# Performance work log

Measured on AMD Instinct MI355X. Metric: run time of the kernel, lower is better.

## Reference

```python
import jax, jax.numpy as jnp
import numpy as np

N_NODES = 50000
N_EDGES = 800000
F_IN = 128
HID = 128
HID4 = HID // 4  # 32
N_SEL = 8192


def gcn_conv(x, src, dst, norm, W, b, n_nodes):
    h = x @ W                              # [N, out]
    msg = h[src] * norm[:, None]           # gather + scale, [E+N, out]
    out = jax.ops.segment_sum(msg, dst, num_segments=n_nodes)  # scatter-add
    return out + b


def setup_inputs() -> dict:
    key = jax.random.key(0)
    ks = jax.random.split(key, 12)
    def glorot(k, shape):
        lim = np.sqrt(6.0 / (shape[0] + shape[1])).astype(np.float32)
        return jax.random.uniform(k, shape, jnp.float32, -lim, lim)
    return {
        "x": jax.random.normal(ks[0], (N_NODES, F_IN), jnp.float32),
        "edge_index": jax.random.randint(ks[1], (2, N_EDGES), 0, N_NODES, jnp.int64 if jax.config.jax_enable_x64 else jnp.int32),
        "relevant_batch_indices": jax.random.randint(ks[2], (N_SEL,), 0, N_NODES),
        "labels": jax.random.randint(ks[3], (N_SEL,), 0, 2),
        "W1": glorot(ks[4], (F_IN, HID)),   "b1": jnp.zeros((HID,), jnp.float32),
        "W2": glorot(ks[5], (HID, HID4)),   "b2": jnp.zeros((HID4,), jnp.float32),
        "W3": glorot(ks[6], (HID4, HID4)),  "b3": jnp.zeros((HID4,), jnp.float32),
        "Wl": glorot(ks[7], (HID4, 2)),     "bl": jnp.zeros((2,), jnp.float32),
    }


def reference(x, edge_index, relevant_batch_indices, labels, W1, b1, W2, b2, W3, b3, Wl, bl):
    n = x.shape[0]
    loops = jnp.arange(n, dtype=edge_index.dtype)
    src = jnp.concatenate([edge_index[0], loops])  # add self-loops
    dst = jnp.concatenate([edge_index[1], loops])
    deg = jax.ops.segment_sum(jnp.ones_like(dst, dtype=x.dtype), dst, num_segments=n)
    dis = jnp.where(deg > 0, jax.lax.rsqrt(jnp.maximum(deg, 1e-12)), 0.0)
    norm = dis[src] * dis[dst]             # [E+N]

    h = jax.nn.relu(gcn_conv(x, src, dst, norm, W1, b1, n))
    h = jax.nn.relu(gcn_conv(h, src, dst, norm, W2, b2, n))
    h = gcn_conv(h, src, dst, norm, W3, b3, n)

    logits = h[relevant_batch_indices] @ Wl + bl   # [N_SEL, 2]
    softmax_vals = jax.nn.softmax(logits, axis=1)
    lsm = jax.nn.log_softmax(logits, axis=1)
    # original slices lsm to labels length if longer; here shapes match
    lsm = lsm[: labels.shape[0]]
    return (lsm, softmax_vals)
```

## Files before the change

kernel.cpp:

```cpp
#include <hip/hip_runtime.h>
#include <hip/hip_fp16.h>

#define F_IN 128
#define HID 128
#define HID4 32
#define NPB 256
#define SRC_BITS 17
#define NBK 256
#define MAXBUCKET 256

static inline size_t alignup(size_t x) { return (x + 255) & ~(size_t)255; }

typedef _Float16 half8 __attribute__((ext_vector_type(8)));
typedef float f32x4 __attribute__((ext_vector_type(4)));

union F4H8 { float4 f; __half2 h[4]; };
union U2H4 { uint2 u; _Float16 h[4]; };


__global__ __launch_bounds__(1024) void hist_k(const int* __restrict__ dst,
                                               int* __restrict__ ghist,
                                               const float* __restrict__ W1,
                                               _Float16* __restrict__ Wt,
                                               int ne, int n_buckets) {
    __shared__ int h[MAXBUCKET];
    const int t = threadIdx.x;
    if (blockIdx.x < 16) {
        int q = blockIdx.x * 1024 + t;
        int k = q >> 7, n = q & 127;
        Wt[n * 128 + k] = (_Float16)W1[q];
    }
    for (int b = t; b < n_buckets; b += 1024) h[b] = 0;
    __syncthreads();
    const int chunk = (ne + NBK - 1) / NBK;
    const int beg = blockIdx.x * chunk;
    const int end = min(ne, beg + chunk);
    for (int e = beg + t; e < end; e += 1024)
        atomicAdd(&h[dst[e] / NPB], 1);
    __syncthreads();
    for (int b = t; b < n_buckets; b += 1024)
        ghist[(size_t)b * NBK + blockIdx.x] = h[b];
}


__global__ void scan_block_k(const int* __restrict__ in, int* __restrict__ out,
                             int* __restrict__ partials, int n) {
    __shared__ int tmp[256];
    int i = blockIdx.x * 256 + threadIdx.x;
    int v = (i < n) ? in[i] : 0;
    tmp[threadIdx.x] = v;
    __syncthreads();
    for (int off = 1; off < 256; off <<= 1) {
        int t = (threadIdx.x >= off) ? tmp[threadIdx.x - off] : 0;
        __syncthreads();
        tmp[threadIdx.x] += t;
        __syncthreads();
    }
    if (i < n) out[i] = tmp[threadIdx.x] - v;
    if (threadIdx.x == 255) partials[blockIdx.x] = tmp[255];
}

__global__ void scan_partials_k(int* __restrict__ partials, int nb) {
    __shared__ int tmp[256];
    int v = (threadIdx.x < nb) ? partials[threadIdx.x] : 0;
    tmp[threadIdx.x] = v;
    __syncthreads();
    for (int off = 1; off < 256; off <<= 1) {
        int t = (threadIdx.x >= off) ? tmp[threadIdx.x - off] : 0;
        __syncthreads();
        tmp[threadIdx.x] += t;
        __syncthreads();
    }
    if (threadIdx.x < nb) partials[threadIdx.x] = tmp[threadIdx.x] - v;
}


__global__ __launch_bounds__(1024) void fused_scatter_gemm1_k(
        const int* __restrict__ src, const int* __restrict__ dst,
        const int* __restrict__ goff, const int* __restrict__ partial2,
        unsigned* __restrict__ tmp, int ne, int n_buckets,
        const float* __restrict__ in, const _Float16* __restrict__ Wt,
        __half* __restrict__ hout, int n_rows) {
    __shared__ int cur[MAXBUCKET];
    __shared__ _Float16 xs[64][136];
    const int t = threadIdx.x;

    if (blockIdx.x < NBK) {
        for (int b = t; b < n_buckets; b += 1024)
            cur[b] = goff[(size_t)b * NBK + blockIdx.x] + partial2[b];
        __syncthreads();
        const int chunk = (ne + NBK - 1) / NBK;
        const int beg = blockIdx.x * chunk;
        const int end = min(ne, beg + chunk);
        for (int e = beg + t; e < end; e += 1024) {
            int d = dst[e];
            int s = src[e];
            int pos = atomicAdd(&cur[d / NPB], 1);
            tmp[pos] = ((unsigned)(d & (NPB - 1)) << SRC_BITS) | (unsigned)s;
        }
        return;
    }

    const int row0 = (blockIdx.x - NBK) * 64;

    #pragma unroll
    for (int i = 0; i < 2; ++i) {
        int q = t + i * 1024;
        int row = q >> 5, c4 = (q & 31) * 4;
        float4 v = make_float4(0.f, 0.f, 0.f, 0.f);
        if (row0 + row < n_rows) v = *(const float4*)(in + (size_t)(row0 + row) * 128 + c4);
        U2H4 cv;
        cv.h[0] = (_Float16)v.x; cv.h[1] = (_Float16)v.y;
        cv.h[2] = (_Float16)v.z; cv.h[3] = (_Float16)v.w;
        *(uint2*)&xs[row][c4] = cv.u;
    }
    __syncthreads();

    const int lane = t & 63;
    const int wave = t >> 6;
    const int r0 = (wave & 3) * 16;
    const int cg = (wave >> 2) * 32;
    const int lrow = lane & 15;
    const int kgrp = (lane >> 4) * 8;

    f32x4 acc[2];
    acc[0] = (f32x4){0.f, 0.f, 0.f, 0.f};
    acc[1] = (f32x4){0.f, 0.f, 0.f, 0.f};

    #pragma unroll
    for (int kk = 0; kk < 4; ++kk) {
        const int k0 = kk * 32 + kgrp;
        half8 a = *(const half8*)&xs[r0 + lrow][k0];
        #pragma unroll
        for (int ct = 0; ct < 2; ++ct) {
            half8 b = *(const half8*)(Wt + (size_t)(cg + ct * 16 + lrow) * 128 + k0);
            acc[ct] = __builtin_amdgcn_mfma_f32_16x16x32_f16(a, b, acc[ct], 0, 0, 0);
        }
    }

    const int rbase = row0 + r0 + (lane >> 4) * 4;
    #pragma unroll
    for (int i = 0; i < 4; ++i) {
        int row = row0 + r0 + (lane >> 4) * 4 + i;
        if (row < n_rows) {
            __half* p = hout + (size_t)row * 128 + cg + lrow;
            p[0]  = __float2half(acc[0][i]);
            p[16] = __float2half(acc[1][i]);
        }
    }
    (void)rbase;
}


__global__ __launch_bounds__(NPB) void binC_k(const unsigned* __restrict__ tmp,
                                              const int* __restrict__ goff,
                                              const int* __restrict__ partial2,
                                              int* __restrict__ deg, float* __restrict__ dis,
                                              int* __restrict__ rowoff, int* __restrict__ csr,
                                              int n_nodes, int ne, int n_buckets) {
    __shared__ int cnt[NPB];
    __shared__ int sc[NPB];
    const int t = threadIdx.x;
    const int bid = blockIdx.x;
    const int base = goff[(size_t)bid * NBK] + partial2[bid];
    const int end = (bid + 1 < n_buckets) ? goff[(size_t)(bid + 1) * NBK] + partial2[bid + 1] : ne;

    cnt[t] = 0;
    __syncthreads();
    for (int j = base + t; j < end; j += NPB)
        atomicAdd(&cnt[tmp[j] >> SRC_BITS], 1);
    __syncthreads();

    int mydeg = cnt[t];
    sc[t] = mydeg;
    __syncthreads();
    for (int off = 1; off < NPB; off <<= 1) {
        int v = (t >= off) ? sc[t - off] : 0;
        __syncthreads();
        sc[t] += v;
        __syncthreads();
    }
    int excl = sc[t] - mydeg;
    int node = bid * NPB + t;
    if (node < n_nodes) {
        deg[node] = mydeg;
        dis[node] = rsqrtf((float)(mydeg + 1));
        rowoff[node] = base + excl;
    }
    cnt[t] = base + excl;
    __syncthreads();
    for (int j = base + t; j < end; j += NPB) {
        unsigned e = tmp[j];
        int ld = e >> SRC_BITS;
        int s  = e & ((1u << SRC_BITS) - 1);
        int pos = atomicAdd(&cnt[ld], 1);
        csr[pos] = s;
    }
}


__global__ void pull1_k(const __half* __restrict__ g, const int* __restrict__ rowoff,
                        const int* __restrict__ deg, const int* __restrict__ csr,
                        const float* __restrict__ dis, const float* __restrict__ b,
                        __half* __restrict__ out, int n_nodes) {
    int gt = blockIdx.x * blockDim.x + threadIdx.x;
    int node = gt >> 4;
    int f0 = (gt & 15) * 8;
    if (node >= n_nodes) return;
    int beg = rowoff[node];
    int end = beg + deg[node];
    float dd = dis[node];

    float acc[8];
    {
        F4H8 v; v.f = *(const float4*)(g + (size_t)node * 128 + f0);
        #pragma unroll
        for (int k = 0; k < 4; ++k) {
            float2 p = __half22float2(v.h[k]);
            acc[2 * k] = dd * p.x; acc[2 * k + 1] = dd * p.y;
        }
    }

    int j = beg;
    for (; j + 2 <= end; j += 2) {
        int s0 = csr[j];
        int s1 = csr[j + 1];
        float w0 = dis[s0];
        float w1 = dis[s1];
        F4H8 v0; v0.f = *(const float4*)(g + (size_t)s0 * 128 + f0);
        F4H8 v1; v1.f = *(const float4*)(g + (size_t)s1 * 128 + f0);
        #pragma unroll
        for (int k = 0; k < 4; ++k) {
            float2 p0 = __half22float2(v0.h[k]);
            float2 p1 = __half22float2(v1.h[k]);
            acc[2 * k]     += w0 * p0.x + w1 * p1.x;
            acc[2 * k + 1] += w0 * p0.y + w1 * p1.y;
        }
    }
    if (j < end) {
        int s = csr[j];
        float w = dis[s];
        F4H8 v; v.f = *(const float4*)(g + (size_t)s * 128 + f0);
        #pragma unroll
        for (int k = 0; k < 4; ++k) {
            float2 p = __half22float2(v.h[k]);
            acc[2 * k] += w * p.x; acc[2 * k + 1] += w * p.y;
        }
    }

    float4 b0 = *(const float4*)(b + f0);
    float4 b1 = *(const float4*)(b + f0 + 4);
    F4H8 o;
    o.h[0] = __floats2half2_rn(fmaxf(b0.x + dd * acc[0], 0.f), fmaxf(b0.y + dd * acc[1], 0.f));
    o.h[1] = __floats2half2_rn(fmaxf(b0.z + dd * acc[2], 0.f), fmaxf(b0.w + dd * acc[3], 0.f));
    o.h[2] = __floats2half2_rn(fmaxf(b1.x + dd * acc[4], 0.f), fmaxf(b1.y + dd * acc[5], 0.f));
    o.h[3] = __floats2half2_rn(fmaxf(b1.z + dd * acc[6], 0.f), fmaxf(b1.w + dd * acc[7], 0.f));
    *(float4*)(out + (size_t)node * 128 + f0) = o.f;
}


__global__ __launch_bounds__(256) void gemm2_k(const __half* __restrict__ in,
                                               const float* __restrict__ W,
                                               const float* __restrict__ dis,
                                               __half* __restrict__ out, int n_rows) {
    __shared__ float xs[64][132];
    __shared__ float wt[128][32];
    const int t = threadIdx.x;
    const int row0 = blockIdx.x * 64;

    #pragma unroll
    for (int i = 0; i < 4; ++i) {
        int q = t + i * 256;
        int row = q >> 4, c8 = (q & 15) * 8;
        F4H8 v;
        v.f = make_float4(0.f, 0.f, 0.f, 0.f);
        if (row0 + row < n_rows)
            v.f = *(const float4*)(in + (size_t)(row0 + row) * 128 + c8);
        #pragma unroll
        for (int k = 0; k < 4; ++k) {
            float2 p = __half22float2(v.h[k]);
            xs[row][c8 + 2 * k] = p.x;
            xs[row][c8 + 2 * k + 1] = p.y;
        }
    }
    #pragma unroll
    for (int i = 0; i < 4; ++i) {
        int q = t + i * 256;
        int kk = q >> 3, c4 = (q & 7) * 4;
        *(float4*)&wt[kk][c4] = *(const float4*)(W + (size_t)kk * 32 + c4);
    }
    __syncthreads();

    const int c4 = (t & 7) * 4;
    const int r2 = (t >> 3) * 2;

    float acc[2][4];
    #pragma unroll
    for (int i = 0; i < 2; ++i)
        #pragma unroll
        for (int j = 0; j < 4; ++j) acc[i][j] = 0.f;

    #pragma unroll 4
    for (int k = 0; k < 128; ++k) {
        float x0 = xs[r2][k], x1 = xs[r2 + 1][k];
        float4 w = *(float4*)&wt[k][c4];
        acc[0][0] += x0 * w.x; acc[0][1] += x0 * w.y; acc[0][2] += x0 * w.z; acc[0][3] += x0 * w.w;
        acc[1][0] += x1 * w.x; acc[1][1] += x1 * w.y; acc[1][2] += x1 * w.z; acc[1][3] += x1 * w.w;
    }

    #pragma unroll
    for (int i = 0; i < 2; ++i) {
        int row = row0 + r2 + i;
        if (row < n_rows) {
            float sc = dis[row];
            U2H4 cv;
            cv.h[0] = (_Float16)(sc * acc[i][0]);
            cv.h[1] = (_Float16)(sc * acc[i][1]);
            cv.h[2] = (_Float16)(sc * acc[i][2]);
            cv.h[3] = (_Float16)(sc * acc[i][3]);
            *(uint2*)(out + (size_t)row * 32 + c4) = cv.u;
        }
    }
}


__global__ void pull2_k(const __half* __restrict__ g, const int* __restrict__ rowoff,
                        const int* __restrict__ deg, const int* __restrict__ csr,
                        const float* __restrict__ dis, const float* __restrict__ b,
                        float* __restrict__ out, int n_nodes) {
    int gt = blockIdx.x * blockDim.x + threadIdx.x;
    int node = gt >> 3;
    int f0 = (gt & 7) * 4;
    if (node >= n_nodes) return;
    int beg = rowoff[node];
    int end = beg + deg[node];
    float dd = dis[node];

    float acc[4];
    {
        U2H4 v; v.u = *(const uint2*)(g + (size_t)node * 32 + f0);
        #pragma unroll
        for (int k = 0; k < 4; ++k) acc[k] = (float)v.h[k];
    }

    int j = beg;
    for (; j + 2 <= end; j += 2) {
        int s0 = csr[j];
        int s1 = csr[j + 1];
        U2H4 v0; v0.u = *(const uint2*)(g + (size_t)s0 * 32 + f0);
        U2H4 v1; v1.u = *(const uint2*)(g + (size_t)s1 * 32 + f0);
        #pragma unroll
        for (int k = 0; k < 4; ++k) acc[k] += (float)v0.h[k] + (float)v1.h[k];
    }
    if (j < end) {
        int s = csr[j];
        U2H4 v; v.u = *(const uint2*)(g + (size_t)s * 32 + f0);
        #pragma unroll
        for (int k = 0; k < 4; ++k) acc[k] += (float)v.h[k];
    }

    float4 bb = *(const float4*)(b + f0);
    *(float4*)(out + (size_t)node * 32 + f0) =
        make_float4(bb.x + dd * acc[0], bb.y + dd * acc[1],
                    bb.z + dd * acc[2], bb.w + dd * acc[3]);
}


__global__ __launch_bounds__(256) void gemm3_k(const float* __restrict__ in,
                                               const float* __restrict__ W,
                                               const float* __restrict__ dis,
                                               float* __restrict__ out, int n_rows) {
    __shared__ float xs[64][36];
    __shared__ float wt[32][32];
    const int t = threadIdx.x;
    const int row0 = blockIdx.x * 64;

    #pragma unroll
    for (int i = 0; i < 2; ++i) {
        int q = t + i * 256;
        int row = q >> 3, c4 = (q & 7) * 4;
        float4 v = make_float4(0.f, 0.f, 0.f, 0.f);
        if (row0 + row < n_rows) {
            v = *(const float4*)(in + (size_t)(row0 + row) * 32 + c4);
            v.x = fmaxf(v.x, 0.f); v.y = fmaxf(v.y, 0.f);
            v.z = fmaxf(v.z, 0.f); v.w = fmaxf(v.w, 0.f);
        }
        *(float4*)&xs[row][c4] = v;
    }
    {
        int kk = t >> 3, c4 = (t & 7) * 4;
        *(float4*)&wt[kk][c4] = *(const float4*)(W + (size_t)kk * 32 + c4);
    }
    __syncthreads();

    const int c4 = (t & 7) * 4;
    const int r2 = (t >> 3) * 2;

    float acc[2][4];
    #pragma unroll
    for (int i = 0; i < 2; ++i)
        #pragma unroll
        for (int j = 0; j < 4; ++j) acc[i][j] = 0.f;

    #pragma unroll
    for (int k = 0; k < 32; ++k) {
        float x0 = xs[r2][k], x1 = xs[r2 + 1][k];
        float4 w = *(float4*)&wt[k][c4];
        acc[0][0] += x0 * w.x; acc[0][1] += x0 * w.y; acc[0][2] += x0 * w.z; acc[0][3] += x0 * w.w;
        acc[1][0] += x1 * w.x; acc[1][1] += x1 * w.y; acc[1][2] += x1 * w.z; acc[1][3] += x1 * w.w;
    }

    #pragma unroll
    for (int i = 0; i < 2; ++i) {
        int row = row0 + r2 + i;
        if (row < n_rows) {
            float sc = dis[row];
            *(float4*)(out + (size_t)row * 32 + c4) =
                make_float4(sc * acc[i][0], sc * acc[i][1], sc * acc[i][2], sc * acc[i][3]);
        }
    }
}


__global__ void pull_head_k(const float* __restrict__ g, const int* __restrict__ rowoff,
                            const int* __restrict__ deg, const int* __restrict__ csr,
                            const float* __restrict__ dis, const float* __restrict__ b3,
                            const int* __restrict__ sel, const float* __restrict__ Wl,
                            const float* __restrict__ bl, float* __restrict__ out, int n_sel) {
    int gt = blockIdx.x * blockDim.x + threadIdx.x;
    int t = gt >> 3;
    int f0 = (gt & 7) * 4;
    if (t >= n_sel) return;
    int node = sel[t];
    int beg = rowoff[node];
    int end = beg + deg[node];
    float dd = dis[node];

    float4 acc = *(const float4*)(g + (size_t)node * 32 + f0);

    int j = beg;
    for (; j + 2 <= end; j += 2) {
        int s0 = csr[j];
        int s1 = csr[j + 1];
        float4 h0 = *(const float4*)(g + (size_t)s0 * 32 + f0);
        float4 h1 = *(const float4*)(g + (size_t)s1 * 32 + f0);
        acc.x += h0.x + h1.x;
        acc.y += h0.y + h1.y;
        acc.z += h0.z + h1.z;
        acc.w += h0.w + h1.w;
    }
    if (j < end) {
        int s = csr[j];
        float4 hs = *(const float4*)(g + (size_t)s * 32 + f0);
        acc.x += hs.x; acc.y += hs.y; acc.z += hs.z; acc.w += hs.w;
    }

    float4 bb = *(const float4*)(b3 + f0);
    float a0 = bb.x + dd * acc.x;
    float a1 = bb.y + dd * acc.y;
    float a2 = bb.z + dd * acc.z;
    float a3 = bb.w + dd * acc.w;

    float l0 = a0 * Wl[(f0 + 0) * 2] + a1 * Wl[(f0 + 1) * 2]
             + a2 * Wl[(f0 + 2) * 2] + a3 * Wl[(f0 + 3) * 2];
    float l1 = a0 * Wl[(f0 + 0) * 2 + 1] + a1 * Wl[(f0 + 1) * 2 + 1]
             + a2 * Wl[(f0 + 2) * 2 + 1] + a3 * Wl[(f0 + 3) * 2 + 1];
    #pragma unroll
    for (int m = 1; m < 8; m <<= 1) {
        l0 += __shfl_xor(l0, m);
        l1 += __shfl_xor(l1, m);
    }
    if ((gt & 7) == 0) {
        l0 += bl[0]; l1 += bl[1];
        float mx = fmaxf(l0, l1);
        float e0 = expf(l0 - mx), e1 = expf(l1 - mx);
        float s = e0 + e1;
        float ls = logf(s);
        *(float2*)(out + (size_t)t * 2) = make_float2((l0 - mx) - ls, (l1 - mx) - ls);
        *(float2*)(out + 2 * (size_t)n_sel + (size_t)t * 2) = make_float2(e0 / s, e1 / s);
    }
}


extern "C" void kernel_launch(void* const* d_in, const int* in_sizes, int n_in,
                              void* d_out, int out_size, void* d_ws, size_t ws_size,
                              hipStream_t stream) {
    const float* x  = (const float*)d_in[0];
    const int* edge = (const int*)d_in[1];
    const int* sel  = (const int*)d_in[2];
    const float* W1 = (const float*)d_in[4];
    const float* b1 = (const float*)d_in[5];
    const float* W2 = (const float*)d_in[6];
    const float* b2 = (const float*)d_in[7];
    const float* W3 = (const float*)d_in[8];
    const float* b3 = (const float*)d_in[9];
    const float* Wl = (const float*)d_in[10];
    const float* bl = (const float*)d_in[11];
    float* out = (float*)d_out;

    const int n_nodes = in_sizes[0] / F_IN;
    const int n_edges = in_sizes[1] / 2;
    const int n_sel   = in_sizes[2];
    const int* srcv = edge;
    const int* dstv = edge + n_edges;
    const int n_buckets = (n_nodes + NPB - 1) / NPB;
    const int n_gh = n_buckets * NBK;

    char* ws = (char*)d_ws;
    int*       deg      = (int*)ws;       ws += alignup((size_t)n_nodes * 4);
    float*     dis      = (float*)ws;     ws += alignup((size_t)n_nodes * 4);
    int*       rowoff   = (int*)ws;       ws += alignup((size_t)n_nodes * 4);
    int*       ghist    = (int*)ws;       ws += alignup((size_t)n_gh * 4);
    int*       goff     = (int*)ws;       ws += alignup((size_t)n_gh * 4);
    int*       partial2 = (int*)ws;       ws += alignup(1024);
    _Float16*  Wt       = (_Float16*)ws;  ws += alignup(128 * 128 * 2);
    unsigned*  tmp      = (unsigned*)ws;  ws += alignup((size_t)n_edges * 4);
    int*       csr      = (int*)ws;       ws += alignup((size_t)n_edges * 4);
    char*      bufA     = ws;             ws += alignup((size_t)n_nodes * HID * 4);
    char*      bufB     = ws;

    const int B = 256;
    #define GRD(n) (((n) + B - 1) / B)
    const int nblk2 = GRD(n_gh);
    const int gemm_blocks = (n_nodes + 63) / 64;

    hist_k<<<NBK, 1024, 0, stream>>>(dstv, ghist, W1, Wt, n_edges, n_buckets);
    scan_block_k<<<nblk2, B, 0, stream>>>(ghist, goff, partial2, n_gh);
    scan_partials_k<<<1, B, 0, stream>>>(partial2, nblk2);

    fused_scatter_gemm1_k<<<NBK + gemm_blocks, 1024, 0, stream>>>(
        srcv, dstv, goff, partial2, tmp, n_edges, n_buckets,
        x, Wt, (__half*)bufA, n_nodes);

    binC_k<<<n_buckets, NPB, 0, stream>>>(tmp, goff, partial2, deg, dis, rowoff, csr,
                                          n_nodes, n_edges, n_buckets);

    pull1_k<<<GRD(n_nodes * 16), B, 0, stream>>>((const __half*)bufA, rowoff, deg, csr,
                                                 dis, b1, (__half*)bufB, n_nodes);

    gemm2_k<<<gemm_blocks, B, 0, stream>>>((const __half*)bufB, W2, dis, (__half*)bufA, n_nodes);
    pull2_k<<<GRD(n_nodes * 8), B, 0, stream>>>((const __half*)bufA, rowoff, deg, csr,
                                                dis, b2, (float*)bufB, n_nodes);

    gemm3_k<<<gemm_blocks, B, 0, stream>>>((const float*)bufB, W3, dis, (float*)bufA, n_nodes);
    pull_head_k<<<GRD(n_sel * 8), B, 0, stream>>>((const float*)bufA, rowoff, deg, csr, dis, b3,
                                                  sel, Wl, bl, out, n_sel);

    #undef GRD
}
```

Measured before the change: 129.3 us.

## Split layer-1 features into four 32-wide slices for cache-friendly gather

Changes the layout of the layer-1 GEMM output from row-major 128-wide rows to four column slices of 32 halves each. The first pull kernel now processes one slice per block and interleaves blocks so that consecutive blocks cover all four slices of nearby node chunks. The aim is a smaller gathered working set per slice (about 3.2 MB instead of 12.8 MB), so the random neighbor reads hit in L2/MALL more often. In exchange each gather is a 64-byte segment instead of a 256-byte row, and the index and degree reads are repeated once per slice. gemm2's loads are updated to read the sliced layout.

```diff
diff --git a/kernel.cpp b/kernel.cpp
--- a/kernel.cpp
+++ b/kernel.cpp
@@ -119,7 +119,7 @@
     const int lane = t & 63;
     const int wave = t >> 6;
     const int r0 = (wave & 3) * 16;
-    const int cg = (wave >> 2) * 32;
+    const int slice = wave >> 2;
     const int lrow = lane & 15;
     const int kgrp = (lane >> 4) * 8;
 
@@ -133,22 +133,20 @@
         half8 a = *(const half8*)&xs[r0 + lrow][k0];
         #pragma unroll
         for (int ct = 0; ct < 2; ++ct) {
-            half8 b = *(const half8*)(Wt + (size_t)(cg + ct * 16 + lrow) * 128 + k0);
+            half8 b = *(const half8*)(Wt + (size_t)(slice * 32 + ct * 16 + lrow) * 128 + k0);
             acc[ct] = __builtin_amdgcn_mfma_f32_16x16x32_f16(a, b, acc[ct], 0, 0, 0);
         }
     }
 
-    const int rbase = row0 + r0 + (lane >> 4) * 4;
     #pragma unroll
     for (int i = 0; i < 4; ++i) {
         int row = row0 + r0 + (lane >> 4) * 4 + i;
         if (row < n_rows) {
-            __half* p = hout + (size_t)row * 128 + cg + lrow;
+            __half* p = hout + ((size_t)slice * n_rows + row) * 32 + lrow;
             p[0]  = __float2half(acc[0][i]);
             p[16] = __float2half(acc[1][i]);
         }
     }
-    (void)rbase;
 }
 
 
@@ -203,17 +201,21 @@
                         const int* __restrict__ deg, const int* __restrict__ csr,
                         const float* __restrict__ dis, const float* __restrict__ b,
                         __half* __restrict__ out, int n_nodes) {
-    int gt = blockIdx.x * blockDim.x + threadIdx.x;
-    int node = gt >> 4;
-    int f0 = (gt & 15) * 8;
+    const int bid = blockIdx.x;
+    const int r = bid & 7;
+    const int slice = r >> 1;
+    const int chunk = (bid >> 3) * 2 + (r & 1);
+    const int node = chunk * 64 + (threadIdx.x >> 2);
     if (node >= n_nodes) return;
+    const int fl = (threadIdx.x & 3) * 8;
+    const __half* gs = g + (size_t)slice * n_nodes * 32;
     int beg = rowoff[node];
     int end = beg + deg[node];
     float dd = dis[node];
 
     float acc[8];
     {
-        F4H8 v; v.f = *(const float4*)(g + (size_t)node * 128 + f0);
+        F4H8 v; v.f = *(const float4*)(gs + (size_t)node * 32 + fl);
         #pragma unroll
         for (int k = 0; k < 4; ++k) {
             float2 p = __half22float2(v.h[k]);
@@ -227,8 +229,8 @@
         int s1 = csr[j + 1];
         float w0 = dis[s0];
         float w1 = dis[s1];
-        F4H8 v0; v0.f = *(const float4*)(g + (size_t)s0 * 128 + f0);
-        F4H8 v1; v1.f = *(const float4*)(g + (size_t)s1 * 128 + f0);
+        F4H8 v0; v0.f = *(const float4*)(gs + (size_t)s0 * 32 + fl);
+        F4H8 v1; v1.f = *(const float4*)(gs + (size_t)s1 * 32 + fl);
         #pragma unroll
         for (int k = 0; k < 4; ++k) {
             float2 p0 = __half22float2(v0.h[k]);
@@ -240,7 +242,7 @@
     if (j < end) {
         int s = csr[j];
         float w = dis[s];
-        F4H8 v; v.f = *(const float4*)(g + (size_t)s * 128 + f0);
+        F4H8 v; v.f = *(const float4*)(gs + (size_t)s * 32 + fl);
         #pragma unroll
         for (int k = 0; k < 4; ++k) {
             float2 p = __half22float2(v.h[k]);
@@ -248,6 +250,7 @@
         }
     }
 
+    const int f0 = slice * 32 + fl;
     float4 b0 = *(const float4*)(b + f0);
     float4 b1 = *(const float4*)(b + f0 + 4);
     F4H8 o;
@@ -255,7 +258,7 @@
     o.h[1] = __floats2half2_rn(fmaxf(b0.z + dd * acc[2], 0.f), fmaxf(b0.w + dd * acc[3], 0.f));
     o.h[2] = __floats2half2_rn(fmaxf(b1.x + dd * acc[4], 0.f), fmaxf(b1.y + dd * acc[5], 0.f));
     o.h[3] = __floats2half2_rn(fmaxf(b1.z + dd * acc[6], 0.f), fmaxf(b1.w + dd * acc[7], 0.f));
-    *(float4*)(out + (size_t)node * 128 + f0) = o.f;
+    *(float4*)(out + ((size_t)slice * n_nodes + node) * 32 + fl) = o.f;
 }
 
 
@@ -271,16 +274,16 @@
     #pragma unroll
     for (int i = 0; i < 4; ++i) {
         int q = t + i * 256;
-        int row = q >> 4, c8 = (q & 15) * 8;
+        int slice = q >> 8, row = (q >> 2) & 63, f8 = (q & 3) * 8;
         F4H8 v;
         v.f = make_float4(0.f, 0.f, 0.f, 0.f);
         if (row0 + row < n_rows)
-            v.f = *(const float4*)(in + (size_t)(row0 + row) * 128 + c8);
+            v.f = *(const float4*)(in + ((size_t)slice * n_rows + row0 + row) * 32 + f8);
         #pragma unroll
         for (int k = 0; k < 4; ++k) {
             float2 p = __half22float2(v.h[k]);
-            xs[row][c8 + 2 * k] = p.x;
-            xs[row][c8 + 2 * k + 1] = p.y;
+            xs[row][slice * 32 + f8 + 2 * k] = p.x;
+            xs[row][slice * 32 + f8 + 2 * k + 1] = p.y;
         }
     }
     #pragma unroll
@@ -523,6 +526,7 @@
     #define GRD(n) (((n) + B - 1) / B)
     const int nblk2 = GRD(n_gh);
     const int gemm_blocks = (n_nodes + 63) / 64;
+    const int chunks = gemm_blocks;
 
     hist_k<<<NBK, 1024, 0, stream>>>(dstv, ghist, W1, Wt, n_edges, n_buckets);
     scan_block_k<<<nblk2, B, 0, stream>>>(ghist, goff, partial2, n_gh);
@@ -535,8 +539,11 @@
     binC_k<<<n_buckets, NPB, 0, stream>>>(tmp, goff, partial2, deg, dis, rowoff, csr,
                                           n_nodes, n_edges, n_buckets);
 
-    pull1_k<<<GRD(n_nodes * 16), B, 0, stream>>>((const __half*)bufA, rowoff, deg, csr,
-                                                 dis, b1, (__half*)bufB, n_nodes);
+    {
+        int g1 = 8 * ((chunks + 1) / 2);
+        pull1_k<<<g1, B, 0, stream>>>((const __half*)bufA, rowoff, deg, csr,
+                                      dis, b1, (__half*)bufB, n_nodes);
+    }
 
     gemm2_k<<<gemm_blocks, B, 0, stream>>>((const __half*)bufB, W2, dis, (__half*)bufA, n_nodes);
     pull2_k<<<GRD(n_nodes * 8), B, 0, stream>>>((const __half*)bufA, rowoff, deg, csr,
```

After: 142.6 us. 10.3% more time.
